# Performance work log

Hardware: AMD Instinct MI355X
Metric: run time of the kernel (lower is better)

The kernel has to match this reference:

```python
import jax, jax.numpy as jnp
import numpy as np

# Grid config (LSS standard, matches init_kwargs)
XB = (-50.0, 50.0, 0.5)
YB = (-50.0, 50.0, 0.5)
ZB = (-10.0, 10.0, 20.0)
DB = (4.0, 45.0, 1.0)
FINAL_DIM = (256, 704)
DOWN = 16
CAMC = 64

DX = jnp.array([XB[2], YB[2], ZB[2]], jnp.float32)
BX = jnp.array([XB[0] + XB[2] / 2.0, YB[0] + YB[2] / 2.0, ZB[0] + ZB[2] / 2.0], jnp.float32)
NX0 = int((XB[1] - XB[0]) / XB[2])  # 200
NX1 = int((YB[1] - YB[0]) / YB[2])  # 200
NZ = int((ZB[1] - ZB[0]) / ZB[2])   # 1


def make_frustum():
    ogfH, ogfW = FINAL_DIM
    fH, fW = ogfH // DOWN, ogfW // DOWN
    ds = jnp.arange(DB[0], DB[1], DB[2], dtype=jnp.float32)  # [D]
    D = ds.shape[0]
    ds = jnp.broadcast_to(ds[:, None, None], (D, fH, fW))
    xs = jnp.broadcast_to(jnp.linspace(0.0, ogfW - 1, fW, dtype=jnp.float32)[None, None, :], (D, fH, fW))
    ys = jnp.broadcast_to(jnp.linspace(0.0, ogfH - 1, fH, dtype=jnp.float32)[None, :, None], (D, fH, fW))
    return jnp.stack((xs, ys, ds), -1)  # [D, fH, fW, 3]


def setup_inputs() -> dict:
    key = jax.random.key(0)
    B, N, D, fH, fW, C = 4, 6, 41, 16, 44, CAMC
    kx, kt = jax.random.split(key, 2)
    x = jax.random.normal(kx, (B, N, D, fH, fW, C), jnp.float32)
    # cam-to-ego base: cam z(forward)->ego x, cam x(right)->-ego y, cam y(down)->-ego z
    base = np.array([[0.0, 0.0, 1.0], [-1.0, 0.0, 0.0], [0.0, -1.0, 0.0]], np.float32)
    yaws = np.linspace(0.0, 2.0 * np.pi, N, endpoint=False).astype(np.float32)
    c, s = np.cos(yaws), np.sin(yaws)
    Rz = np.zeros((N, 3, 3), np.float32)
    Rz[:, 0, 0] = c; Rz[:, 0, 1] = -s; Rz[:, 1, 0] = s; Rz[:, 1, 1] = c; Rz[:, 2, 2] = 1.0
    rots_np = np.einsum('nij,jk->nik', Rz, base)
    rots = jnp.asarray(np.tile(rots_np[None], (B, 1, 1, 1)))
    # pinhole intrinsics for 704x256 image
    K = np.array([[550.0, 0.0, 352.0], [0.0, 550.0, 128.0], [0.0, 0.0, 1.0]], np.float32)
    intrins = jnp.asarray(np.tile(K[None, None], (B, N, 1, 1)))
    post_rots = jnp.asarray(np.tile(np.eye(3, dtype=np.float32)[None, None], (B, N, 1, 1)))
    post_trans = jnp.zeros((B, N, 3), jnp.float32)
    trans = jax.random.uniform(kt, (B, N, 3), jnp.float32, -1.5, 1.5)
    return {"x": x, "rots": rots, "trans": trans, "intrins": intrins,
            "post_rots": post_rots, "post_trans": post_trans}


def _forward(x, rots, trans, intrins, post_rots, post_trans):
    B, N, D, fH, fW, C = x.shape
    frustum = make_frustum()  # [D,fH,fW,3]

    # ---- get_geometry ----
    intrins_inv = jnp.linalg.inv(intrins)        # [B,N,3,3]
    post_rots_inv = jnp.linalg.inv(post_rots)    # [B,N,3,3]
    cam_to_ego = rots @ intrins_inv              # [B,N,3,3]
    pts = frustum[None, None] - post_trans[:, :, None, None, None, :]        # [B,N,D,fH,fW,3]
    # points @ post_rots_inv^T  ==  post_rots_inv @ points
    pts = jnp.einsum('bndhwc,bnkc->bndhwk', pts, post_rots_inv)
    pts = jnp.concatenate([pts[..., :2] * pts[..., 2:3], pts[..., 2:3]], -1)
    geom = jnp.einsum('bndhwc,bnkc->bndhwk', pts, cam_to_ego) + trans[:, :, None, None, None, :]

    # ---- voxel_pooling ----
    Nprime = B * N * D * fH * fW
    feats = x.reshape(Nprime, C)
    g = (geom - (BX - DX / 2.0)) / DX
    g = jnp.clip(g, -1e6, 1e6)
    g = jnp.trunc(g).astype(jnp.int32).reshape(Nprime, 3)  # torch .long() truncates toward zero
    batch_ix = jnp.repeat(jnp.arange(B, dtype=jnp.int32), Nprime // B)
    kept = ((g[:, 0] >= 0) & (g[:, 0] < NX0) &
            (g[:, 1] >= 0) & (g[:, 1] < NX1) &
            (g[:, 2] >= 0) & (g[:, 2] < NZ))
    # flat index into [B, NZ, NX0, NX1]; sort+cumsum_trick+scatter == segment-sum per voxel
    idx = batch_ix * (NZ * NX0 * NX1) + g[:, 2] * (NX0 * NX1) + g[:, 0] * NX1 + g[:, 1]
    idx = jnp.where(kept, idx, 0)
    w = kept.astype(feats.dtype)[:, None]
    pooled = jax.ops.segment_sum(feats * w, idx, num_segments=B * NZ * NX0 * NX1)
    final = pooled.reshape(B, NZ, NX0, NX1, C)
    # torch.cat(final.unbind(dim=2), 1) on [B,C,NZ,X,Y] -> [B, NZ*C, X, Y] (z-major)
    final = jnp.transpose(final, (0, 1, 4, 2, 3)).reshape(B, NZ * C, NX0, NX1)
    return final


def reference(x, rots, trans, intrins, post_rots, post_trans):
    return _forward(x, rots, trans, intrins, post_rots, post_trans)
```

## Files before the change

kernel.cpp:

```cpp
#include <hip/hip_runtime.h>
#include <cstddef>

#define NB   4
#define NN_  6
#define ND_  41
#define NFH  16
#define NFW  44
#define NC   64
#define NX0_ 200
#define NX1_ 200
#define NXY  (NX0_ * NX1_)
#define NCOL (NB * NN_ * ND_ * NFW)

__device__ __forceinline__ void inv3(const float* a, float* inv) {
    float c00 = __fsub_rn(__fmul_rn(a[4], a[8]), __fmul_rn(a[5], a[7]));
    float c01 = __fsub_rn(__fmul_rn(a[5], a[6]), __fmul_rn(a[3], a[8]));
    float c02 = __fsub_rn(__fmul_rn(a[3], a[7]), __fmul_rn(a[4], a[6]));
    float det = __fadd_rn(__fadd_rn(__fmul_rn(a[0], c00), __fmul_rn(a[1], c01)),
                          __fmul_rn(a[2], c02));
    inv[0] = __fdiv_rn(c00, det);
    inv[1] = __fdiv_rn(__fsub_rn(__fmul_rn(a[2], a[7]), __fmul_rn(a[1], a[8])), det);
    inv[2] = __fdiv_rn(__fsub_rn(__fmul_rn(a[1], a[5]), __fmul_rn(a[2], a[4])), det);
    inv[3] = __fdiv_rn(c01, det);
    inv[4] = __fdiv_rn(__fsub_rn(__fmul_rn(a[0], a[8]), __fmul_rn(a[2], a[6])), det);
    inv[5] = __fdiv_rn(__fsub_rn(__fmul_rn(a[2], a[3]), __fmul_rn(a[0], a[5])), det);
    inv[6] = __fdiv_rn(c02, det);
    inv[7] = __fdiv_rn(__fsub_rn(__fmul_rn(a[1], a[6]), __fmul_rn(a[0], a[7])), det);
    inv[8] = __fdiv_rn(__fsub_rn(__fmul_rn(a[0], a[4]), __fmul_rn(a[1], a[3])), det);
}

__global__ void setup_kernel(const float* __restrict__ rots,
                             const float* __restrict__ trans,
                             const float* __restrict__ intrins,
                             const float* __restrict__ post_rots,
                             const float* __restrict__ post_trans,
                             float* __restrict__ mats) {
    int t = threadIdx.x;
    if (t >= NB * NN_) return;
    const float* R  = rots      + t * 9;
    const float* K  = intrins   + t * 9;
    const float* PR = post_rots + t * 9;
    float Kinv[9], Pinv[9];
    inv3(K, Kinv);
    inv3(PR, Pinv);
    float* o = mats + t * 24;
    for (int i = 0; i < 3; ++i)
        for (int k = 0; k < 3; ++k) {
            float s = __fmul_rn(R[i * 3 + 0], Kinv[0 * 3 + k]);
            s = __fadd_rn(s, __fmul_rn(R[i * 3 + 1], Kinv[1 * 3 + k]));
            s = __fadd_rn(s, __fmul_rn(R[i * 3 + 2], Kinv[2 * 3 + k]));
            o[i * 3 + k] = s;
        }
    for (int i = 0; i < 9; ++i) o[9 + i] = Pinv[i];
    o[18] = trans[t * 3 + 0];
    o[19] = trans[t * 3 + 1];
    o[20] = trans[t * 3 + 2];
    o[21] = post_trans[t * 3 + 0];
    o[22] = post_trans[t * 3 + 1];
    o[23] = post_trans[t * 3 + 2];
}

__device__ __forceinline__ void hw_fadd(float* p, float v) {
    asm volatile("global_atomic_add_f32 %0, %1, off" : : "v"(p), "v"(v) : "memory");
}

__device__ __forceinline__ int compute_idx(int b, int n, int d, int h, int w,
                                           const float* __restrict__ mats) {
    const float* mp = mats + (b * NN_ + n) * 24;

    float u   = (w == NFW - 1) ? 703.0f : (float)((double)w * (703.0 / 43.0));
    float v   = __fmul_rn((float)h, 17.0f);
    float dep = (float)(4 + d);

    float f0 = __fsub_rn(u, mp[21]);
    float f1 = __fsub_rn(v, mp[22]);
    float f2 = __fsub_rn(dep, mp[23]);

    float q0 = __fadd_rn(__fadd_rn(__fmul_rn(mp[9],  f0), __fmul_rn(mp[10], f1)), __fmul_rn(mp[11], f2));
    float q1 = __fadd_rn(__fadd_rn(__fmul_rn(mp[12], f0), __fmul_rn(mp[13], f1)), __fmul_rn(mp[14], f2));
    float q2 = __fadd_rn(__fadd_rn(__fmul_rn(mp[15], f0), __fmul_rn(mp[16], f1)), __fmul_rn(mp[17], f2));

    float r0 = __fmul_rn(q0, q2);
    float r1 = __fmul_rn(q1, q2);

    float g0 = __fadd_rn(__fadd_rn(__fadd_rn(__fmul_rn(mp[0], r0), __fmul_rn(mp[1], r1)), __fmul_rn(mp[2], q2)), mp[18]);
    float g1 = __fadd_rn(__fadd_rn(__fadd_rn(__fmul_rn(mp[3], r0), __fmul_rn(mp[4], r1)), __fmul_rn(mp[5], q2)), mp[19]);
    float g2 = __fadd_rn(__fadd_rn(__fadd_rn(__fmul_rn(mp[6], r0), __fmul_rn(mp[7], r1)), __fmul_rn(mp[8], q2)), mp[20]);

    float s0 = __fdiv_rn(__fsub_rn(g0, -50.0f), 0.5f);
    float s1 = __fdiv_rn(__fsub_rn(g1, -50.0f), 0.5f);
    float s2 = __fdiv_rn(__fsub_rn(g2, -10.0f), 20.0f);
    s0 = fminf(fmaxf(s0, -1e6f), 1e6f);
    s1 = fminf(fmaxf(s1, -1e6f), 1e6f);
    s2 = fminf(fmaxf(s2, -1e6f), 1e6f);
    int i0 = (int)s0;
    int i1 = (int)s1;
    int i2 = (int)s2;
    if (i0 >= 0 && i0 < NX0_ && i1 >= 0 && i1 < NX1_ && i2 >= 0 && i2 < 1)
        return b * NXY + i0 * NX1_ + i1;
    return -1;
}

template <bool TO_WS>
__global__ __launch_bounds__(256) void col_pool(const float* __restrict__ x,
                                                const float* __restrict__ mats,
                                                float* __restrict__ dst) {
    int cid = blockIdx.x * 8 + (threadIdx.x >> 5);
    int sub = threadIdx.x & 31;
    int l   = sub & 15;
    int hh  = sub >> 4;
    int w = cid % NFW; int t = cid / NFW;
    int d = t % ND_;   t /= ND_;
    int n = t % NN_;   int b = t / NN_;

    int myidx = compute_idx(b, n, d, l, w, mats);

    int vmin = (myidx >= 0) ? myidx : 0x7fffffff;
    int vmax = myidx;
    #pragma unroll
    for (int k = 1; k < 16; k <<= 1) {
        vmin = min(vmin, __shfl_xor(vmin, k, 16));
        vmax = max(vmax, __shfl_xor(vmax, k, 16));
    }
    if (vmax < 0) return;
    int  common  = vmax;
    bool allsame = (vmin == vmax) || (vmin == 0x7fffffff);

    int idx8[8];
    #pragma unroll
    for (int j = 0; j < 8; ++j) idx8[j] = __shfl(myidx, hh * 8 + j, 32);

    const float4* xp = (const float4*)
        (x + (((size_t)((b * NN_ + n) * ND_ + d) * NFH) * NFW + w) * NC) + l;
    const int HSTRIDE = NFW * (NC / 4);

    float4 v[8];
    #pragma unroll
    for (int j = 0; j < 8; ++j) v[j] = xp[(hh * 8 + j) * HSTRIDE];

    if (__builtin_expect(allsame, 1)) {
        float4 a0 = make_float4(0.f, 0.f, 0.f, 0.f);
        float4 a1 = make_float4(0.f, 0.f, 0.f, 0.f);
        #pragma unroll
        for (int j = 0; j < 8; j += 2) {
            float m0 = (idx8[j]     >= 0) ? 1.0f : 0.0f;
            float m1 = (idx8[j + 1] >= 0) ? 1.0f : 0.0f;
            a0.x += v[j].x * m0;     a0.y += v[j].y * m0;
            a0.z += v[j].z * m0;     a0.w += v[j].w * m0;
            a1.x += v[j + 1].x * m1; a1.y += v[j + 1].y * m1;
            a1.z += v[j + 1].z * m1; a1.w += v[j + 1].w * m1;
        }
        a0.x += a1.x; a0.y += a1.y; a0.z += a1.z; a0.w += a1.w;
        a0.x += __shfl_xor(a0.x, 16, 32);
        a0.y += __shfl_xor(a0.y, 16, 32);
        a0.z += __shfl_xor(a0.z, 16, 32);
        a0.w += __shfl_xor(a0.w, 16, 32);
        if (hh == 0) {
            if (TO_WS) {
                float* o = dst + (size_t)common * NC + (l << 2);
                hw_fadd(o,     a0.x);
                hw_fadd(o + 1, a0.y);
                hw_fadd(o + 2, a0.z);
                hw_fadd(o + 3, a0.w);
            } else {
                int bb = common / NXY, xy = common % NXY;
                float* o = dst + ((size_t)(bb * NC + l * 4)) * NXY + xy;
                hw_fadd(o,           a0.x);
                hw_fadd(o + NXY,     a0.y);
                hw_fadd(o + 2 * NXY, a0.z);
                hw_fadd(o + 3 * NXY, a0.w);
            }
        }
    } else {
        #pragma unroll
        for (int j = 0; j < 8; ++j) {
            if (idx8[j] >= 0) {
                if (TO_WS) {
                    float* o = dst + (size_t)idx8[j] * NC + (l << 2);
                    hw_fadd(o,     v[j].x);
                    hw_fadd(o + 1, v[j].y);
                    hw_fadd(o + 2, v[j].z);
                    hw_fadd(o + 3, v[j].w);
                } else {
                    int bb = idx8[j] / NXY, xy = idx8[j] % NXY;
                    float* o = dst + ((size_t)(bb * NC + l * 4)) * NXY + xy;
                    hw_fadd(o,           v[j].x);
                    hw_fadd(o + NXY,     v[j].y);
                    hw_fadd(o + 2 * NXY, v[j].z);
                    hw_fadd(o + 3 * NXY, v[j].w);
                }
            }
        }
    }
}

__global__ __launch_bounds__(256) void transpose_ws(const float* __restrict__ ws,
                                                    float* __restrict__ out) {
    __shared__ float4 tile[64 * 16];
    int b   = blockIdx.y;
    int xy0 = blockIdx.x * 64;

    const float4* src = (const float4*)(ws + ((size_t)b * NXY + xy0) * NC);
    #pragma unroll
    for (int s = 0; s < 4; ++s) {
        int f  = s * 256 + threadIdx.x;
        int i  = f >> 4;
        int c4 = f & 15;
        tile[i * 16 + (c4 ^ ((i >> 2) & 15))] = src[f];
    }
    __syncthreads();

    int l  = threadIdx.x & 63;
    int wv = threadIdx.x >> 6;
    int q  = l & 15;
    int lh = l >> 4;
    int i0 = q << 2;
    #pragma unroll
    for (int s = 0; s < 4; ++s) {
        int c  = s * 16 + wv * 4 + lh;
        int c4 = c >> 2, cr = c & 3;
        float4 v;
        v.x = ((const float*)&tile[(i0 + 0) * 16 + (c4 ^ q)])[cr];
        v.y = ((const float*)&tile[(i0 + 1) * 16 + (c4 ^ q)])[cr];
        v.z = ((const float*)&tile[(i0 + 2) * 16 + (c4 ^ q)])[cr];
        v.w = ((const float*)&tile[(i0 + 3) * 16 + (c4 ^ q)])[cr];
        *(float4*)(out + ((size_t)(b * NC + c)) * NXY + xy0 + i0) = v;
    }
}

extern "C" void kernel_launch(void* const* d_in, const int* in_sizes, int n_in,
                              void* d_out, int out_size, void* d_ws, size_t ws_size,
                              hipStream_t stream) {
    (void)in_sizes; (void)n_in; (void)out_size;
    const float* x          = (const float*)d_in[0];
    const float* rots       = (const float*)d_in[1];
    const float* trans      = (const float*)d_in[2];
    const float* intrins    = (const float*)d_in[3];
    const float* post_rots  = (const float*)d_in[4];
    const float* post_trans = (const float*)d_in[5];
    float* out = (float*)d_out;

    const size_t acc_floats = (size_t)NB * NXY * NC;
    const size_t need = (acc_floats + 1024) * sizeof(float);

    if (ws_size >= need) {
        float* acc  = (float*)d_ws;
        float* mats = acc + acc_floats;
        setup_kernel<<<1, 32, 0, stream>>>(rots, trans, intrins, post_rots, post_trans, mats);
        hipMemsetAsync(acc, 0, acc_floats * sizeof(float), stream);
        col_pool<true><<<NCOL / 8, 256, 0, stream>>>(x, mats, acc);
        transpose_ws<<<dim3(NXY / 64, NB), 256, 0, stream>>>(acc, out);
    } else {
        float* mats = (float*)d_ws;
        setup_kernel<<<1, 32, 0, stream>>>(rots, trans, intrins, post_rots, post_trans, mats);
        hipMemsetAsync(out, 0, (size_t)NB * NC * NXY * sizeof(float), stream);
        col_pool<false><<<NCOL / 8, 256, 0, stream>>>(x, mats, out);
    }
}
```

Measured before the change: 280.5 us.

## Split pooling into metadata pass and per-slice column-sum scatter kernel

Adds a separate kernel that computes, for each image column, its target voxel cell and a 16-bit validity mask. A new scatter kernel then works on one depth slice per 704-thread block: each thread sums all 16 rows for its float4 channel chunk and issues a single atomic add. The old kernel split each column's rows across two half-warps and combined them with shuffles. Each thread now does more serial loading, and the extra launch adds overhead. Mixed-cell columns are recomputed per row inside the scatter kernel, and the fallback path gets a simplified direct kernel.

```diff
diff --git a/kernel.cpp b/kernel.cpp
--- a/kernel.cpp
+++ b/kernel.cpp
@@ -11,6 +11,7 @@
 #define NX1_ 200
 #define NXY  (NX0_ * NX1_)
 #define NCOL (NB * NN_ * ND_ * NFW)
+#define NSLICE (NB * NN_ * ND_)
 
 __device__ __forceinline__ void inv3(const float* a, float* inv) {
     float c00 = __fsub_rn(__fmul_rn(a[4], a[8]), __fmul_rn(a[5], a[7]));
@@ -101,94 +102,104 @@
     return -1;
 }
 
-template <bool TO_WS>
-__global__ __launch_bounds__(256) void col_pool(const float* __restrict__ x,
-                                                const float* __restrict__ mats,
-                                                float* __restrict__ dst) {
-    int cid = blockIdx.x * 8 + (threadIdx.x >> 5);
-    int sub = threadIdx.x & 31;
-    int l   = sub & 15;
-    int hh  = sub >> 4;
+__global__ __launch_bounds__(256) void build_meta(const float* __restrict__ mats,
+                                                  int2* __restrict__ colmeta) {
+    int cid = blockIdx.x * 16 + (threadIdx.x >> 4);
+    int l   = threadIdx.x & 15;
     int w = cid % NFW; int t = cid / NFW;
     int d = t % ND_;   t /= ND_;
     int n = t % NN_;   int b = t / NN_;
 
     int myidx = compute_idx(b, n, d, l, w, mats);
 
+    int vm   = (myidx >= 0) ? (1 << l) : 0;
     int vmin = (myidx >= 0) ? myidx : 0x7fffffff;
     int vmax = myidx;
     #pragma unroll
     for (int k = 1; k < 16; k <<= 1) {
+        vm  |= __shfl_xor(vm,  k, 16);
         vmin = min(vmin, __shfl_xor(vmin, k, 16));
         vmax = max(vmax, __shfl_xor(vmax, k, 16));
     }
-    if (vmax < 0) return;
-    int  common  = vmax;
-    bool allsame = (vmin == vmax) || (vmin == 0x7fffffff);
-
-    int idx8[8];
-    #pragma unroll
-    for (int j = 0; j < 8; ++j) idx8[j] = __shfl(myidx, hh * 8 + j, 32);
-
-    const float4* xp = (const float4*)
-        (x + (((size_t)((b * NN_ + n) * ND_ + d) * NFH) * NFW + w) * NC) + l;
-    const int HSTRIDE = NFW * (NC / 4);
-
-    float4 v[8];
-    #pragma unroll
-    for (int j = 0; j < 8; ++j) v[j] = xp[(hh * 8 + j) * HSTRIDE];
-
-    if (__builtin_expect(allsame, 1)) {
-        float4 a0 = make_float4(0.f, 0.f, 0.f, 0.f);
-        float4 a1 = make_float4(0.f, 0.f, 0.f, 0.f);
+    if (l == 0) {
+        int cell;
+        if (vmax < 0)            { cell = -1; vm = 0; }
+        else if (vmin == vmax)   { cell = vmax; }
+        else                     { cell = -3; }
+        colmeta[cid] = make_int2(cell, vm);
+    }
+}
+
+__global__ __launch_bounds__(704) void colsum_scatter(const float* __restrict__ x,
+                                                      const int2* __restrict__ colmeta,
+                                                      const float* __restrict__ mats,
+                                                      float* __restrict__ acc) {
+    __shared__ int2 smeta[NFW];
+    int slice = blockIdx.x;
+    int t = threadIdx.x;
+    if (t < NFW) smeta[t] = colmeta[slice * NFW + t];
+    __syncthreads();
+
+    int w  = t >> 4;
+    int c4 = t & 15;
+    int2 meta = smeta[w];
+    int cell = meta.x;
+    unsigned vm = (unsigned)meta.y;
+    bool multi = (cell == -3);
+    if (vm == 0 && !multi) return;
+
+    const float4* xp = (const float4*)(x + (size_t)slice * (NFH * NFW * NC)) + t;
+    const int RS = NFW * (NC / 4);
+
+    if (__builtin_expect(!multi, 1)) {
+        float4 v[8];
+        float4 A0 = make_float4(0.f, 0.f, 0.f, 0.f);
+        float4 A1 = make_float4(0.f, 0.f, 0.f, 0.f);
+        #pragma unroll
+        for (int j = 0; j < 8; ++j) v[j] = xp[j * RS];
         #pragma unroll
         for (int j = 0; j < 8; j += 2) {
-            float m0 = (idx8[j]     >= 0) ? 1.0f : 0.0f;
-            float m1 = (idx8[j + 1] >= 0) ? 1.0f : 0.0f;
-            a0.x += v[j].x * m0;     a0.y += v[j].y * m0;
-            a0.z += v[j].z * m0;     a0.w += v[j].w * m0;
-            a1.x += v[j + 1].x * m1; a1.y += v[j + 1].y * m1;
-            a1.z += v[j + 1].z * m1; a1.w += v[j + 1].w * m1;
-        }
-        a0.x += a1.x; a0.y += a1.y; a0.z += a1.z; a0.w += a1.w;
-        a0.x += __shfl_xor(a0.x, 16, 32);
-        a0.y += __shfl_xor(a0.y, 16, 32);
-        a0.z += __shfl_xor(a0.z, 16, 32);
-        a0.w += __shfl_xor(a0.w, 16, 32);
-        if (hh == 0) {
-            if (TO_WS) {
-                float* o = dst + (size_t)common * NC + (l << 2);
-                hw_fadd(o,     a0.x);
-                hw_fadd(o + 1, a0.y);
-                hw_fadd(o + 2, a0.z);
-                hw_fadd(o + 3, a0.w);
-            } else {
-                int bb = common / NXY, xy = common % NXY;
-                float* o = dst + ((size_t)(bb * NC + l * 4)) * NXY + xy;
-                hw_fadd(o,           a0.x);
-                hw_fadd(o + NXY,     a0.y);
-                hw_fadd(o + 2 * NXY, a0.z);
-                hw_fadd(o + 3 * NXY, a0.w);
-            }
-        }
+            float m0 = ((vm >> j) & 1) ? 1.0f : 0.0f;
+            float m1 = ((vm >> (j + 1)) & 1) ? 1.0f : 0.0f;
+            A0.x += v[j].x * m0;     A0.y += v[j].y * m0;
+            A0.z += v[j].z * m0;     A0.w += v[j].w * m0;
+            A1.x += v[j + 1].x * m1; A1.y += v[j + 1].y * m1;
+            A1.z += v[j + 1].z * m1; A1.w += v[j + 1].w * m1;
+        }
+        float4 s0 = make_float4(A0.x + A1.x, A0.y + A1.y, A0.z + A1.z, A0.w + A1.w);
+
+        float4 B0 = make_float4(0.f, 0.f, 0.f, 0.f);
+        float4 B1 = make_float4(0.f, 0.f, 0.f, 0.f);
+        #pragma unroll
+        for (int j = 0; j < 8; ++j) v[j] = xp[(8 + j) * RS];
+        #pragma unroll
+        for (int j = 0; j < 8; j += 2) {
+            float m0 = ((vm >> (8 + j)) & 1) ? 1.0f : 0.0f;
+            float m1 = ((vm >> (9 + j)) & 1) ? 1.0f : 0.0f;
+            B0.x += v[j].x * m0;     B0.y += v[j].y * m0;
+            B0.z += v[j].z * m0;     B0.w += v[j].w * m0;
+            B1.x += v[j + 1].x * m1; B1.y += v[j + 1].y * m1;
+            B1.z += v[j + 1].z * m1; B1.w += v[j + 1].w * m1;
+        }
+        float4 s1 = make_float4(B0.x + B1.x, B0.y + B1.y, B0.z + B1.z, B0.w + B1.w);
+
+        float* o = acc + (size_t)cell * NC + (c4 << 2);
+        hw_fadd(o,     s0.x + s1.x);
+        hw_fadd(o + 1, s0.y + s1.y);
+        hw_fadd(o + 2, s0.z + s1.z);
+        hw_fadd(o + 3, s0.w + s1.w);
     } else {
-        #pragma unroll
-        for (int j = 0; j < 8; ++j) {
-            if (idx8[j] >= 0) {
-                if (TO_WS) {
-                    float* o = dst + (size_t)idx8[j] * NC + (l << 2);
-                    hw_fadd(o,     v[j].x);
-                    hw_fadd(o + 1, v[j].y);
-                    hw_fadd(o + 2, v[j].z);
-                    hw_fadd(o + 3, v[j].w);
-                } else {
-                    int bb = idx8[j] / NXY, xy = idx8[j] % NXY;
-                    float* o = dst + ((size_t)(bb * NC + l * 4)) * NXY + xy;
-                    hw_fadd(o,           v[j].x);
-                    hw_fadd(o + NXY,     v[j].y);
-                    hw_fadd(o + 2 * NXY, v[j].z);
-                    hw_fadd(o + 3 * NXY, v[j].w);
-                }
+        int d = slice % ND_; int r = slice / ND_;
+        int n = r % NN_;     int b = r / NN_;
+        for (int h = 0; h < 16; ++h) {
+            int ch = compute_idx(b, n, d, h, w, mats);
+            if (ch >= 0) {
+                float4 vv = xp[h * RS];
+                float* o = acc + (size_t)ch * NC + (c4 << 2);
+                hw_fadd(o,     vv.x);
+                hw_fadd(o + 1, vv.y);
+                hw_fadd(o + 2, vv.z);
+                hw_fadd(o + 3, vv.w);
             }
         }
     }
@@ -225,6 +236,44 @@
         v.z = ((const float*)&tile[(i0 + 2) * 16 + (c4 ^ q)])[cr];
         v.w = ((const float*)&tile[(i0 + 3) * 16 + (c4 ^ q)])[cr];
         *(float4*)(out + ((size_t)(b * NC + c)) * NXY + xy0 + i0) = v;
+    }
+}
+
+__global__ __launch_bounds__(256) void col_pool_direct(const float* __restrict__ x,
+                                                       const float* __restrict__ mats,
+                                                       float* __restrict__ dst) {
+    int cid = blockIdx.x * 8 + (threadIdx.x >> 5);
+    int sub = threadIdx.x & 31;
+    int l   = sub & 15;
+    int hh  = sub >> 4;
+    int w = cid % NFW; int t = cid / NFW;
+    int d = t % ND_;   t /= ND_;
+    int n = t % NN_;   int b = t / NN_;
+
+    int myidx = compute_idx(b, n, d, l, w, mats);
+    int idx8[8];
+    #pragma unroll
+    for (int j = 0; j < 8; ++j) idx8[j] = __shfl(myidx, hh * 8 + j, 32);
+
+    int vmax = myidx;
+    #pragma unroll
+    for (int k = 1; k < 16; k <<= 1) vmax = max(vmax, __shfl_xor(vmax, k, 16));
+    if (vmax < 0) return;
+
+    const float4* xp = (const float4*)
+        (x + (((size_t)((b * NN_ + n) * ND_ + d) * NFH) * NFW + w) * NC) + l;
+    const int HSTRIDE = NFW * (NC / 4);
+    #pragma unroll
+    for (int j = 0; j < 8; ++j) {
+        if (idx8[j] >= 0) {
+            float4 v = xp[(hh * 8 + j) * HSTRIDE];
+            int bb = idx8[j] / NXY, xy = idx8[j] % NXY;
+            float* o = dst + ((size_t)(bb * NC + l * 4)) * NXY + xy;
+            hw_fadd(o,           v.x);
+            hw_fadd(o + NXY,     v.y);
+            hw_fadd(o + 2 * NXY, v.z);
+            hw_fadd(o + 3 * NXY, v.w);
+        }
     }
 }
 
@@ -241,19 +290,21 @@
     float* out = (float*)d_out;
 
     const size_t acc_floats = (size_t)NB * NXY * NC;
-    const size_t need = (acc_floats + 1024) * sizeof(float);
+    const size_t need = (acc_floats + (size_t)NCOL * 2 + 1024) * sizeof(float);
 
     if (ws_size >= need) {
-        float* acc  = (float*)d_ws;
-        float* mats = acc + acc_floats;
+        float* acc     = (float*)d_ws;
+        int2*  colmeta = (int2*)(acc + acc_floats);
+        float* mats    = (float*)(colmeta + NCOL);
         setup_kernel<<<1, 32, 0, stream>>>(rots, trans, intrins, post_rots, post_trans, mats);
         hipMemsetAsync(acc, 0, acc_floats * sizeof(float), stream);
-        col_pool<true><<<NCOL / 8, 256, 0, stream>>>(x, mats, acc);
+        build_meta<<<NCOL / 16, 256, 0, stream>>>(mats, colmeta);
+        colsum_scatter<<<NSLICE, 704, 0, stream>>>(x, colmeta, mats, acc);
         transpose_ws<<<dim3(NXY / 64, NB), 256, 0, stream>>>(acc, out);
     } else {
         float* mats = (float*)d_ws;
         setup_kernel<<<1, 32, 0, stream>>>(rots, trans, intrins, post_rots, post_trans, mats);
         hipMemsetAsync(out, 0, (size_t)NB * NC * NXY * sizeof(float), stream);
-        col_pool<false><<<NCOL / 8, 256, 0, stream>>>(x, mats, out);
-    }
-}
+        col_pool_direct<<<NCOL / 8, 256, 0, stream>>>(x, mats, out);
+    }
+}
```

Measured after the change: 288.2 us. 2.7% more time.
